# Kernel tuning notes

Measured on AMD Instinct MI355X. Metric: run time of the kernel, lower is better.

The kernel has to match this reference:

```python
import jax, jax.numpy as jnp
import numpy as np

SCALE = 8.0  # sqrt(head_dim=64); module divides scores by self.scale


def setup_inputs() -> dict:
    key = jax.random.key(0)
    kq, kk, kv = jax.random.split(key, 3)
    B, H, L, D = 4, 8, 2048, 64
    queries = jax.random.normal(kq, (B, H, L, D), dtype=jnp.float32)
    keys = jax.random.normal(kk, (B, H, L, D), dtype=jnp.float32)
    values = jax.random.normal(kv, (B, H, L, D), dtype=jnp.float32)
    return {"queries": queries, "keys": keys, "values": values}


def reference(queries, keys, values):
    # scores: [B, H, L_Q, L_K]
    L_Q, L_K = queries.shape[2], keys.shape[2]
    scores = jnp.einsum('bnqd,bnkd->bnqk', queries, keys) / SCALE
    # causal mask: triu(ones, diagonal=1) positions set to -inf
    causal = jnp.triu(jnp.ones((L_Q, L_K), dtype=bool), k=1)
    scores = jnp.where(causal[None, None, :, :], -jnp.inf, scores)
    A = jax.nn.softmax(scores, axis=-1)  # dropout p=0.0 (eval) -> identity
    V = jnp.einsum('bnqk,bnkd->bnqd', A, values)
    return V
```

## Files before the change

### kernel.cpp

```cpp
#include <hip/hip_runtime.h>
#include <hip/hip_bf16.h>

typedef __attribute__((ext_vector_type(8))) short bf16x8;
typedef __attribute__((ext_vector_type(16))) float f32x16;

#define DHEAD 64
#define L_SEQ 2048
#define QSCALE (0.125f * 1.44269504088896340736f)

#define WS_ML_OFF   4096
#define WS_PART_OFF (4096 + 2048 * 128 * 8)
#define WS_NEED     ((size_t)WS_PART_OFF + (size_t)768 * 128 * 64 * 2)

union U4S8 { uint4 u; bf16x8 s; };

__device__ __forceinline__ unsigned pk2(float a, float b) {
    unsigned r;
    asm("v_cvt_pk_bf16_f32 %0, %1, %2" : "=v"(r) : "v"(a), "v"(b));
    return r;
}
__device__ __forceinline__ float bfrt(float x) {
    return __uint_as_float(pk2(x, x) << 16);
}
__device__ __forceinline__ float bf2f(unsigned short u) {
    return __uint_as_float((unsigned)u << 16);
}

__device__ __forceinline__ float fexp2(float x) {
#if __has_builtin(__builtin_amdgcn_exp2f)
    return __builtin_amdgcn_exp2f(x);
#else
    return __expf(x * 0.69314718055994530942f);
#endif
}

#define MAX16(P) fmaxf(fmaxf(fmaxf(fmaxf(P[0],P[1]),fmaxf(P[2],P[3])),          \
                             fmaxf(fmaxf(P[4],P[5]),fmaxf(P[6],P[7]))),         \
                       fmaxf(fmaxf(fmaxf(P[8],P[9]),fmaxf(P[10],P[11])),        \
                             fmaxf(fmaxf(P[12],P[13]),fmaxf(P[14],P[15]))))
#define SUM16(P) ((((P[0]+P[1])+(P[2]+P[3]))+((P[4]+P[5])+(P[6]+P[7])))         \
                + (((P[8]+P[9])+(P[10]+P[11]))+((P[12]+P[13])+(P[14]+P[15]))))


__constant__ unsigned char JOBS[40] = {
    (15<<2)|0, (15<<2)|1, (15<<2)|2, (15<<2)|3,
    (14<<2)|0, (14<<2)|1, (14<<2)|2,
    (13<<2)|0, (13<<2)|1, (13<<2)|2,
    (12<<2)|0, (12<<2)|1, (12<<2)|2,
    (11<<2)|0, (11<<2)|1, (11<<2)|2,
    (10<<2)|0, (10<<2)|1,
    ( 9<<2)|0, ( 9<<2)|1,
    ( 8<<2)|0, ( 8<<2)|1,
    ( 7<<2)|0, ( 7<<2)|1,
    ( 6<<2)|0, ( 5<<2)|0, ( 4<<2)|0, ( 3<<2)|0,
    (14<<2)|3, (10<<2)|2, ( 6<<2)|1, ( 2<<2)|0,
    (13<<2)|3, ( 9<<2)|2, ( 5<<2)|1, ( 1<<2)|0,
    (12<<2)|3, ( 8<<2)|2, ( 4<<2)|1, ( 0<<2)|0,
};

template<int MODE>
__global__ __launch_bounds__(256, 3)
void fattn_kernel(const float* __restrict__ Qg, const float* __restrict__ Kg,
                  const float* __restrict__ Vg, float* __restrict__ Og,
                  char* __restrict__ wsBase) {
    __shared__ uint4 sK4[8][64];
    __shared__ uint4 sV4[8][64];

    const int tid  = threadIdx.x;
    const int lane = tid & 63;
    const int w    = tid >> 6;
    const int hi   = lane >> 5;
    const int c    = lane & 31;

    const int id  = blockIdx.x;
    const int bh  = (id & 7) + 8 * ((id >> 3) & 3);

    int T, sg, t0, te;
    if (MODE == 2) {
        const unsigned jb = JOBS[id >> 5];
        T  = jb >> 2;
        sg = jb & 3;
        t0 = 8 * sg;
        te = 2 * T + 1; if (te > t0 + 7) te = t0 + 7;
    } else {
        const int u_ = id >> 5;
        T = (u_ < 8) ? (15 - u_) : (u_ - 8);
        sg = 0; t0 = 0; te = 2 * T + 1;
    }

    const size_t base = (size_t)bh * L_SEQ * DHEAD;
    const int q0w = T * 128 + w * 32;

    bf16x8 qf[4];
    {
        const float* Qrow = Qg + base + (size_t)(q0w + c) * DHEAD;
        #pragma unroll
        for (int kc = 0; kc < 4; ++kc) {
            float4 aa = *(const float4*)(Qrow + kc * 16 + hi * 8);
            float4 bb = *(const float4*)(Qrow + kc * 16 + hi * 8 + 4);
            U4S8 t;
            t.u = make_uint4(pk2(aa.x * QSCALE, aa.y * QSCALE),
                             pk2(aa.z * QSCALE, aa.w * QSCALE),
                             pk2(bb.x * QSCALE, bb.y * QSCALE),
                             pk2(bb.z * QSCALE, bb.w * QSCALE));
            qf[kc] = t.s;
        }
    }

    const float* Kpb = Kg + base + (size_t)(32 * (w & 1) + c) * DHEAD
                          + (w >> 1) * 32 + hi * 8;
    const float* Vpb = Vg + base + (size_t)(16 * w + 8 * hi) * DHEAD + c;
    const int kch = (w & 1) * 4 + (w >> 1) * 2;
    const int ksl = hi * 32 + c;

    auto stage64 = [&](int t64) {
        const float* Kp = Kpb + (size_t)t64 * 64 * DHEAD;
        float4 k0 = *(const float4*)(Kp + 0);
        float4 k1 = *(const float4*)(Kp + 4);
        float4 k2 = *(const float4*)(Kp + 16);
        float4 k3 = *(const float4*)(Kp + 20);
        sK4[kch][ksl]     = make_uint4(pk2(k0.x, k0.y), pk2(k0.z, k0.w),
                                       pk2(k1.x, k1.y), pk2(k1.z, k1.w));
        sK4[kch + 1][ksl] = make_uint4(pk2(k2.x, k2.y), pk2(k2.z, k2.w),
                                       pk2(k3.x, k3.y), pk2(k3.z, k3.w));
        const float* Vp = Vpb + (size_t)t64 * 64 * DHEAD;
        float a0 = Vp[0 * DHEAD], a1 = Vp[1 * DHEAD], a2 = Vp[2 * DHEAD], a3 = Vp[3 * DHEAD];
        float a4 = Vp[4 * DHEAD], a5 = Vp[5 * DHEAD], a6 = Vp[6 * DHEAD], a7 = Vp[7 * DHEAD];
        sV4[w * 2][ksl] = make_uint4(pk2(a0, a1), pk2(a2, a3), pk2(a4, a5), pk2(a6, a7));
        a0 = Vp[0 * DHEAD + 32]; a1 = Vp[1 * DHEAD + 32]; a2 = Vp[2 * DHEAD + 32];
        a3 = Vp[3 * DHEAD + 32]; a4 = Vp[4 * DHEAD + 32]; a5 = Vp[5 * DHEAD + 32];
        a6 = Vp[6 * DHEAD + 32]; a7 = Vp[7 * DHEAD + 32];
        sV4[w * 2 + 1][ksl] = make_uint4(pk2(a0, a1), pk2(a2, a3), pk2(a4, a5), pk2(a6, a7));
    };

    f32x16 o0 = {0,0,0,0,0,0,0,0,0,0,0,0,0,0,0,0};
    f32x16 o1 = o0;
    float m_r = -1e30f, l_r = 0.f;

    stage64(t0);
    __syncthreads();

    for (int t64 = t0; t64 <= te; ++t64) {
        const int lim = 4 * T + w - 2 * t64 + 1;
        const int nkb = lim < 0 ? 0 : (lim > 2 ? 2 : lim);

        if (nkb > 0) {
            float p[2][16];

            __builtin_amdgcn_s_setprio(1);
            #pragma unroll
            for (int i = 0; i < 2; ++i) {
                if (i < nkb) {
                    f32x16 s = {0,0,0,0,0,0,0,0,0,0,0,0,0,0,0,0};
                    #pragma unroll
                    for (int kc = 0; kc < 4; ++kc) {
                        U4S8 t; t.u = sK4[i * 4 + kc][lane];
                        s = __builtin_amdgcn_mfma_f32_32x32x16_bf16(t.s, qf[kc], s, 0, 0, 0);
                    }
                    #pragma unroll
                    for (int r = 0; r < 16; ++r) p[i][r] = s[r];
                }
            }
            __builtin_amdgcn_s_setprio(0);

            #pragma unroll
            for (int i = 0; i < 2; ++i) {
                if (2 * t64 + i == 4 * T + w) {
                    #pragma unroll
                    for (int r = 0; r < 16; ++r) {
                        const int kk = (r & 3) + 8 * (r >> 2) + 4 * hi;
                        if (kk > c) p[i][r] = -1e30f;
                    }
                }
            }

            float mx = MAX16(p[0]);
            if (nkb > 1) mx = fmaxf(mx, MAX16(p[1]));
            mx = fmaxf(mx, __shfl_xor(mx, 32));

            if (__any(mx > m_r + 8.f)) {
                const float mn    = fmaxf(m_r, mx);
                const float alpha = fexp2(m_r - mn);
                m_r  = mn;
                l_r *= alpha;
                #pragma unroll
                for (int r = 0; r < 16; ++r) {
                    const float ab = __shfl(alpha, (r & 3) + 8 * (r >> 2) + 4 * hi);
                    o0[r] *= ab; o1[r] *= ab;
                }
            }

            #pragma unroll
            for (int i = 0; i < 2; ++i) {
                if (i < nkb) {
                    #pragma unroll
                    for (int r = 0; r < 16; ++r) p[i][r] = fexp2(p[i][r] - m_r);
                }
            }
            float rs = SUM16(p[0]);
            if (nkb > 1) rs += SUM16(p[1]);
            rs += __shfl_xor(rs, 32);
            l_r += rs;

            __builtin_amdgcn_s_setprio(1);
            #pragma unroll
            for (int kcl = 0; kcl < 4; ++kcl) {
                if (kcl < 2 * nkb) {
                    const int i = kcl >> 1, bs = (kcl & 1) * 8;
                    unsigned a0 = pk2(p[i][bs + 0], p[i][bs + 1]);
                    unsigned a1 = pk2(p[i][bs + 2], p[i][bs + 3]);
                    unsigned b0 = pk2(p[i][bs + 4], p[i][bs + 5]);
                    unsigned b1 = pk2(p[i][bs + 6], p[i][bs + 7]);
                    asm("v_permlane32_swap_b32 %0, %1" : "+v"(a0), "+v"(b0));
                    asm("v_permlane32_swap_b32 %0, %1" : "+v"(a1), "+v"(b1));
                    U4S8 t;
                    t.u = make_uint4(a0, a1, b0, b1);
                    U4S8 tv0; tv0.u = sV4[kcl * 2][lane];
                    o0 = __builtin_amdgcn_mfma_f32_32x32x16_bf16(t.s, tv0.s, o0, 0, 0, 0);
                    U4S8 tv1; tv1.u = sV4[kcl * 2 + 1][lane];
                    o1 = __builtin_amdgcn_mfma_f32_32x32x16_bf16(t.s, tv1.s, o1, 0, 0, 0);
                }
            }
            __builtin_amdgcn_s_setprio(0);
        }

        if (t64 < te) {
            __syncthreads();
            stage64(t64 + 1);
            __syncthreads();
        }
    }

    float* Op = Og + base;

    if (MODE == 0 || T <= 3) {
        const float linv = 1.f / l_r;
        #pragma unroll
        for (int r = 0; r < 16; ++r) {
            const int   cr  = (r & 3) + 8 * (r >> 2) + 4 * hi;
            const float lb  = __shfl(linv, cr);
            const int   row = q0w + cr;
            Op[(size_t)row * DHEAD + c]      = o0[r] * lb;
            Op[(size_t)row * DHEAD + 32 + c] = o1[r] * lb;
        }
        return;
    }

    const int f4 = (bh * 16 + T) * 4;
    float2* ml = (float2*)(wsBase + WS_ML_OFF);
    if (hi == 0) ml[(size_t)(f4 + sg) * 128 + w * 32 + c] = make_float2(m_r, l_r);
    if (sg == 0) {
        #pragma unroll
        for (int r = 0; r < 16; ++r) {
            const int cr  = (r & 3) + 8 * (r >> 2) + 4 * hi;
            const int row = q0w + cr;
            Op[(size_t)row * DHEAD + c]      = bfrt(o0[r]);
            Op[(size_t)row * DHEAD + 32 + c] = bfrt(o1[r]);
        }
    } else {
        const int g  = T >> 2;
        const int ps = bh * 24 + 2 * g * (g - 1) + (T & 3) * g + (sg - 1);
        unsigned short* mp = (unsigned short*)(wsBase + WS_PART_OFF) + (size_t)ps * 128 * 64;
        #pragma unroll
        for (int r = 0; r < 16; ++r) {
            const int cr   = (r & 3) + 8 * (r >> 2) + 4 * hi;
            const int lrow = w * 32 + cr;
            mp[lrow * 64 + c]      = (unsigned short)pk2(o0[r], o0[r]);
            mp[lrow * 64 + 32 + c] = (unsigned short)pk2(o1[r], o1[r]);
        }
    }
}

__global__ __launch_bounds__(256)
void merge_kernel(float* __restrict__ Og, const char* __restrict__ wsBase) {
    const int blk = blockIdx.x;
    const int bh = blk >> 4, T = blk & 15;
    if (T <= 3) return;
    const int n  = (T >> 2) + 1;
    const int f4 = (bh * 16 + T) * 4;
    const int g  = T >> 2;
    const int psb = bh * 24 + 2 * g * (g - 1) + (T & 3) * g;

    const float2* ml = (const float2*)(wsBase + WS_ML_OFF);
    const unsigned short* part = (const unsigned short*)(wsBase + WS_PART_OFF);
    const unsigned short* p1 = part + (size_t)(psb + 0) * 128 * 64;
    const unsigned short* p2 = part + (size_t)(psb + 1) * 128 * 64;
    const unsigned short* p3 = part + (size_t)(psb + 2) * 128 * 64;
    float* Op = Og + ((size_t)bh * L_SEQ + (size_t)T * 128) * DHEAD;

    __shared__ float sA0[128], sA1[128], sA2[128], sA3[128], sLi[128];
    const int t = threadIdx.x;
    if (t < 128) {
        const float2 m0 = ml[(size_t)(f4 + 0) * 128 + t];
        const float2 m1 = ml[(size_t)(f4 + 1) * 128 + t];
        const float2 m2 = (n > 2) ? ml[(size_t)(f4 + 2) * 128 + t] : make_float2(-1e30f, 0.f);
        const float2 m3 = (n > 3) ? ml[(size_t)(f4 + 3) * 128 + t] : make_float2(-1e30f, 0.f);
        const float mM = fmaxf(fmaxf(m0.x, m1.x), fmaxf(m2.x, m3.x));
        const float a0 = fexp2(m0.x - mM), a1 = fexp2(m1.x - mM);
        const float a2 = fexp2(m2.x - mM), a3 = fexp2(m3.x - mM);
        sA0[t] = a0; sA1[t] = a1; sA2[t] = a2; sA3[t] = a3;
        sLi[t] = 1.f / (a0 * m0.y + a1 * m1.y + a2 * m2.y + a3 * m3.y);
    }
    __syncthreads();

    #pragma unroll
    for (int e = 0; e < 8; ++e) {
        const int idx4 = e * 256 + t;
        const int row  = idx4 >> 4;
        const int c4   = (idx4 & 15) * 4;
        const int off  = row * 64 + c4;
        const float a0 = sA0[row], li = sLi[row];
        float4 po = *(float4*)&Op[off];
        po.x *= a0; po.y *= a0; po.z *= a0; po.w *= a0;
        {
            const float a1 = sA1[row];
            const ushort4 u = *(const ushort4*)&p1[off];
            po.x += a1 * bf2f(u.x); po.y += a1 * bf2f(u.y);
            po.z += a1 * bf2f(u.z); po.w += a1 * bf2f(u.w);
        }
        if (n > 2) {
            const float a2 = sA2[row];
            const ushort4 u = *(const ushort4*)&p2[off];
            po.x += a2 * bf2f(u.x); po.y += a2 * bf2f(u.y);
            po.z += a2 * bf2f(u.z); po.w += a2 * bf2f(u.w);
        }
        if (n > 3) {
            const float a3 = sA3[row];
            const ushort4 u = *(const ushort4*)&p3[off];
            po.x += a3 * bf2f(u.x); po.y += a3 * bf2f(u.y);
            po.z += a3 * bf2f(u.z); po.w += a3 * bf2f(u.w);
        }
        po.x *= li; po.y *= li; po.z *= li; po.w *= li;
        *(float4*)&Op[off] = po;
    }
}

extern "C" void kernel_launch(void* const* d_in, const int* in_sizes, int n_in,
                              void* d_out, int out_size, void* d_ws, size_t ws_size,
                              hipStream_t stream) {
    const float* Q = (const float*)d_in[0];
    const float* K = (const float*)d_in[1];
    const float* V = (const float*)d_in[2];
    float* O = (float*)d_out;
    if (ws_size >= WS_NEED) {
        fattn_kernel<2><<<dim3(1280), dim3(256), 0, stream>>>(Q, K, V, O, (char*)d_ws);
        merge_kernel<<<dim3(512), dim3(256), 0, stream>>>(O, (const char*)d_ws);
    } else {
        fattn_kernel<0><<<dim3(512), dim3(256), 0, stream>>>(Q, K, V, O, (char*)d_ws);
    }
}
```

Before: 55.03 us.

## Double-buffer K/V shared tiles with register prefetch of next tile

K/V staging now goes through two LDS buffers. The next tile's global loads are issued into registers before computing on the current tile, then converted and written to the other buffer afterwards, which drops one barrier per iteration. This is meant to hide global load latency behind the MFMA work. It adds 32 VGPRs of prefetch state and doubles LDS use, which may pressure occupancy under launch_bounds(256,3).

```diff
diff --git a/kernel.cpp b/kernel.cpp
--- a/kernel.cpp
+++ b/kernel.cpp
@@ -63,8 +63,8 @@
 void fattn_kernel(const float* __restrict__ Qg, const float* __restrict__ Kg,
                   const float* __restrict__ Vg, float* __restrict__ Og,
                   char* __restrict__ wsBase) {
-    __shared__ uint4 sK4[8][64];
-    __shared__ uint4 sV4[8][64];
+    __shared__ uint4 sK4[2][8][64];
+    __shared__ uint4 sV4[2][8][64];
 
     const int tid  = threadIdx.x;
     const int lane = tid & 63;
@@ -113,34 +113,47 @@
     const int kch = (w & 1) * 4 + (w >> 1) * 2;
     const int ksl = hi * 32 + c;
 
-    auto stage64 = [&](int t64) {
+    float4 rk[4];
+    float  rv[16];
+
+    auto load_tile = [&](int t64) {
         const float* Kp = Kpb + (size_t)t64 * 64 * DHEAD;
-        float4 k0 = *(const float4*)(Kp + 0);
-        float4 k1 = *(const float4*)(Kp + 4);
-        float4 k2 = *(const float4*)(Kp + 16);
-        float4 k3 = *(const float4*)(Kp + 20);
-        sK4[kch][ksl]     = make_uint4(pk2(k0.x, k0.y), pk2(k0.z, k0.w),
-                                       pk2(k1.x, k1.y), pk2(k1.z, k1.w));
-        sK4[kch + 1][ksl] = make_uint4(pk2(k2.x, k2.y), pk2(k2.z, k2.w),
-                                       pk2(k3.x, k3.y), pk2(k3.z, k3.w));
+        rk[0] = *(const float4*)(Kp + 0);
+        rk[1] = *(const float4*)(Kp + 4);
+        rk[2] = *(const float4*)(Kp + 16);
+        rk[3] = *(const float4*)(Kp + 20);
         const float* Vp = Vpb + (size_t)t64 * 64 * DHEAD;
-        float a0 = Vp[0 * DHEAD], a1 = Vp[1 * DHEAD], a2 = Vp[2 * DHEAD], a3 = Vp[3 * DHEAD];
-        float a4 = Vp[4 * DHEAD], a5 = Vp[5 * DHEAD], a6 = Vp[6 * DHEAD], a7 = Vp[7 * DHEAD];
-        sV4[w * 2][ksl] = make_uint4(pk2(a0, a1), pk2(a2, a3), pk2(a4, a5), pk2(a6, a7));
-        a0 = Vp[0 * DHEAD + 32]; a1 = Vp[1 * DHEAD + 32]; a2 = Vp[2 * DHEAD + 32];
-        a3 = Vp[3 * DHEAD + 32]; a4 = Vp[4 * DHEAD + 32]; a5 = Vp[5 * DHEAD + 32];
-        a6 = Vp[6 * DHEAD + 32]; a7 = Vp[7 * DHEAD + 32];
-        sV4[w * 2 + 1][ksl] = make_uint4(pk2(a0, a1), pk2(a2, a3), pk2(a4, a5), pk2(a6, a7));
+        #pragma unroll
+        for (int j = 0; j < 8; ++j) {
+            rv[j]     = Vp[j * DHEAD];
+            rv[8 + j] = Vp[j * DHEAD + 32];
+        }
+    };
+
+    auto write_tile = [&](int nb) {
+        sK4[nb][kch][ksl]     = make_uint4(pk2(rk[0].x, rk[0].y), pk2(rk[0].z, rk[0].w),
+                                           pk2(rk[1].x, rk[1].y), pk2(rk[1].z, rk[1].w));
+        sK4[nb][kch + 1][ksl] = make_uint4(pk2(rk[2].x, rk[2].y), pk2(rk[2].z, rk[2].w),
+                                           pk2(rk[3].x, rk[3].y), pk2(rk[3].z, rk[3].w));
+        sV4[nb][w * 2][ksl]     = make_uint4(pk2(rv[0], rv[1]),  pk2(rv[2], rv[3]),
+                                             pk2(rv[4], rv[5]),  pk2(rv[6], rv[7]));
+        sV4[nb][w * 2 + 1][ksl] = make_uint4(pk2(rv[8], rv[9]),  pk2(rv[10], rv[11]),
+                                             pk2(rv[12], rv[13]), pk2(rv[14], rv[15]));
     };
 
     f32x16 o0 = {0,0,0,0,0,0,0,0,0,0,0,0,0,0,0,0};
     f32x16 o1 = o0;
     float m_r = -1e30f, l_r = 0.f;
 
-    stage64(t0);
+    load_tile(t0);
+    write_tile(0);
     __syncthreads();
 
     for (int t64 = t0; t64 <= te; ++t64) {
+        const int  cur = (t64 - t0) & 1;
+        const bool pf  = (t64 < te);
+        if (pf) load_tile(t64 + 1);
+
         const int lim = 4 * T + w - 2 * t64 + 1;
         const int nkb = lim < 0 ? 0 : (lim > 2 ? 2 : lim);
 
@@ -154,7 +167,7 @@
                     f32x16 s = {0,0,0,0,0,0,0,0,0,0,0,0,0,0,0,0};
                     #pragma unroll
                     for (int kc = 0; kc < 4; ++kc) {
-                        U4S8 t; t.u = sK4[i * 4 + kc][lane];
+                        U4S8 t; t.u = sK4[cur][i * 4 + kc][lane];
                         s = __builtin_amdgcn_mfma_f32_32x32x16_bf16(t.s, qf[kc], s, 0, 0, 0);
                     }
                     #pragma unroll
@@ -215,18 +228,17 @@
                     asm("v_permlane32_swap_b32 %0, %1" : "+v"(a1), "+v"(b1));
                     U4S8 t;
                     t.u = make_uint4(a0, a1, b0, b1);
-                    U4S8 tv0; tv0.u = sV4[kcl * 2][lane];
+                    U4S8 tv0; tv0.u = sV4[cur][kcl * 2][lane];
                     o0 = __builtin_amdgcn_mfma_f32_32x32x16_bf16(t.s, tv0.s, o0, 0, 0, 0);
-                    U4S8 tv1; tv1.u = sV4[kcl * 2 + 1][lane];
+                    U4S8 tv1; tv1.u = sV4[cur][kcl * 2 + 1][lane];
                     o1 = __builtin_amdgcn_mfma_f32_32x32x16_bf16(t.s, tv1.s, o1, 0, 0, 0);
                 }
             }
             __builtin_amdgcn_s_setprio(0);
         }
 
-        if (t64 < te) {
-            __syncthreads();
-            stage64(t64 + 1);
+        if (pf) {
+            write_tile(cur ^ 1);
             __syncthreads();
         }
     }
```

Result: no change. 55.81 us (+1.4%).
